# Optimization experiments

Measured on AMD Instinct MI355X. Metric: run time of the kernel, lower is better.

Reference implementation:

```python
import jax, jax.numpy as jnp
import numpy as np

B, MAXN, D, H, S = 64, 512, 512, 8, 32
DH = D // H          # per-head dim = 64
N = B * MAXN         # 32768 total nodes
E = 524288           # ~avg degree 16
EPS = 1e-5


def setup_inputs() -> dict:
    key = jax.random.key(0)
    ks = jax.random.split(key, 18)
    s = 0.05
    x_dense = jax.random.normal(ks[0], (B, MAXN, D), jnp.float32)
    x = jax.random.normal(ks[1], (N, D), jnp.float32)
    src = jax.random.randint(ks[2], (E,), 0, N)
    # destinations kept within the same graph as the source
    dst = (src // MAXN) * MAXN + jax.random.randint(ks[3], (E,), 0, MAXN)
    edge_index = jnp.stack([src, dst]).astype(jnp.int32)
    batch = (jnp.arange(N) // MAXN).astype(jnp.int32)  # sorted, 512 nodes/graph
    seed = jax.random.normal(ks[4], (S, 1, D), jnp.float32) * s
    # per-head GCN conv weights concatenated along output dim: [D, H*DH] == [D, D]
    Wk = jax.random.normal(ks[5], (D, D), jnp.float32) * s
    bk = jnp.zeros((D,), jnp.float32)
    Wv = jax.random.normal(ks[6], (D, D), jnp.float32) * s
    bv = jnp.zeros((D,), jnp.float32)
    q_proj_weight = jax.random.normal(ks[7], (D, D), jnp.float32) * s
    Wo = jax.random.normal(ks[8], (D, D), jnp.float32) * s
    bo = jnp.zeros((D,), jnp.float32)
    Wff = jax.random.normal(ks[9], (D, D), jnp.float32) * s
    bff = jnp.zeros((D,), jnp.float32)
    gamma_h = jnp.ones((D,), jnp.float32)
    beta_h = jnp.zeros((D,), jnp.float32)
    gamma_z = jnp.ones((D,), jnp.float32)
    beta_z = jnp.zeros((D,), jnp.float32)
    return dict(x_dense=x_dense, x=x, edge_index=edge_index, batch=batch,
                seed=seed, Wk=Wk, bk=bk, Wv=Wv, bv=bv,
                q_proj_weight=q_proj_weight, Wo=Wo, bo=bo, Wff=Wff, bff=bff,
                gamma_h=gamma_h, beta_h=beta_h, gamma_z=gamma_z, beta_z=beta_z)


def _gcn(x, W, b, src, dst):
    # PyG GCNConv with self-loops + symmetric norm; all H heads fused via W [D, H*DH]
    xw = x @ W                                   # [N, D]
    idx = jnp.arange(N)
    src_f = jnp.concatenate([src, idx])
    dst_f = jnp.concatenate([dst, idx])
    deg = jax.ops.segment_sum(jnp.ones_like(dst_f, dtype=x.dtype), dst_f, num_segments=N)
    dinv = jax.lax.rsqrt(deg)                    # deg >= 1 (self-loops)
    norm = dinv[src_f] * dinv[dst_f]             # [E+N]
    out = jax.ops.segment_sum(xw[src_f] * norm[:, None], dst_f, num_segments=N)
    return out + b


def _to_dense(feat, batch):
    # to_dense_batch for sorted batch vector; padded slots are zeros
    counts = jax.ops.segment_sum(jnp.ones((N,), jnp.int32), batch, num_segments=B)
    start = jnp.cumsum(counts) - counts
    pos = jnp.arange(N) - start[batch]
    return jnp.zeros((B, MAXN, feat.shape[-1]), feat.dtype).at[batch, pos].set(feat)


def _layernorm(x, g, b):
    m = jnp.mean(x, -1, keepdims=True)
    v = jnp.mean(jnp.square(x - m), -1, keepdims=True)
    return (x - m) * jax.lax.rsqrt(v + EPS) * g + b


def reference(x_dense, x, edge_index, batch, seed, Wk, bk, Wv, bv,
              q_proj_weight, Wo, bo, Wff, bff, gamma_h, beta_h, gamma_z, beta_z):
    src, dst = edge_index[0], edge_index[1]
    k_nodes = _gcn(x, Wk, bk, src, dst)          # [N, D] (H heads concat)
    v_nodes = _gcn(x, Wv, bv, src, dst)
    k_dense = _to_dense(k_nodes, batch)          # [B, MAXN, D]
    v_dense = _to_dense(v_nodes, batch)

    # query: seed [S,1,D] repeated over batch -> [S,B,D]; q projection (F.linear)
    query = jnp.broadcast_to(seed, (S, B, D))
    q = jnp.einsum('sbd,ed->sbe', query, q_proj_weight)
    scale = 1.0 / jnp.sqrt(jnp.float32(DH))
    qh = (q * scale).reshape(S, B, H, DH).transpose(1, 2, 0, 3)     # [B,H,S,DH]
    kh = k_dense.reshape(B, MAXN, H, DH).transpose(0, 2, 1, 3)      # [B,H,N,DH]
    vh = v_dense.reshape(B, MAXN, H, DH).transpose(0, 2, 1, 3)
    scores = jnp.einsum('bhsd,bhnd->bhsn', qh, kh)                  # [B,H,S,MAXN]
    attn = jax.nn.softmax(scores, axis=-1)                          # no padding mask (faithful)
    ctx = jnp.einsum('bhsn,bhnd->bhsd', attn, vh)                   # [B,H,S,DH]
    ctx = ctx.transpose(0, 2, 1, 3).reshape(B, S, D)                # heads concat
    attn_out = ctx @ Wo.T + bo                                      # [B,S,D]

    query_bse = jnp.broadcast_to(seed.transpose(1, 0, 2), (B, S, D))
    embed = _layernorm(query_bse + attn_out, gamma_h, beta_h)
    embed = _layernorm(embed + embed @ Wff.T + bff, gamma_z, beta_z)
    return embed
```

## Files before the change

kernel.cpp:

```cpp
#include <hip/hip_runtime.h>
#include <hip/hip_bf16.h>

#define BN   64
#define MAXN 512
#define DIM  512
#define NH   8
#define NS   32
#define NN   32768
#define NE   524288
#define NBLK 256
#define EPB  (NE / NBLK)
#define MP   (2048 * 512)

typedef __hip_bfloat16 bf16;
using bf16x8 = __attribute__((ext_vector_type(8))) short;
using f32x4  = __attribute__((ext_vector_type(4))) float;

__device__ int            g_cnt[NN];
__device__ int            g_off[NN + 1];
__device__ int            g_csr[NE];
__device__ unsigned short g_hist[(long)NBLK * NN];
__device__ unsigned short g_bpfx[(long)NBLK * NN];
__device__ float g_dinv[NN];
__device__ bf16  g_xb[NN * DIM];
__device__ bf16  g_agg[NN * DIM];
__device__ bf16  g_aggT[NN * DIM];
__device__ bf16  g_qf[256 * DIM];
__device__ bf16  g_wob[DIM * DIM];
__device__ bf16  g_wvb[DIM * DIM];
__device__ bf16  g_wvo[DIM * 8 * DIM];
__device__ float g_bvo[DIM];
__device__ bf16  g_wffT[DIM * DIM];
__device__ float g_q[NS * DIM];
__device__ bf16  g_sc[BN * 256 * MAXN];
__device__ bf16  g_cp[BN * NS * 8 * DIM];
__device__ float g_part[4 * MP];
__device__ float g_h1[BN * NS * DIM];
__device__ bf16  g_h1b[BN * NS * DIM];

__device__ inline float bf2f(unsigned short u) {
    union { unsigned int i; float f; } x; x.i = ((unsigned int)u) << 16; return x.f;
}

__device__ inline void gll16(const bf16* g, bf16* l) {
    __builtin_amdgcn_global_load_lds(
        (const __attribute__((address_space(1))) void*)g,
        (__attribute__((address_space(3))) void*)l, 16, 0, 0);
}

__global__ __launch_bounds__(1024) void k_hist(const int* __restrict__ dst) {
    __shared__ unsigned int h[NN];
    int p = blockIdx.x, tid = threadIdx.x;
    for (int i = tid; i < NN / 4; i += 1024) ((int4*)h)[i] = make_int4(0, 0, 0, 0);
    __syncthreads();
#pragma unroll
    for (int j = 0; j < EPB / 1024; j++) {
        int e = p * EPB + j * 1024 + tid;
        atomicAdd(&h[dst[e]], 1u);
    }
    __syncthreads();
    unsigned int* out32 = (unsigned int*)(g_hist + (long)p * NN);
    for (int i = tid; i < NN / 2; i += 1024)
        out32[i] = h[2 * i] | (h[2 * i + 1] << 16);
}

__global__ __launch_bounds__(256) void k_colscan() {
    int v2 = blockIdx.x * 256 + threadIdx.x;
    const unsigned int* H = (const unsigned int*)g_hist;
    unsigned int* B = (unsigned int*)g_bpfx;
    unsigned int s0 = 0, s1 = 0;
#pragma unroll 8
    for (int p = 0; p < NBLK; p++) {
        unsigned int hh = H[(long)p * (NN / 2) + v2];
        B[(long)p * (NN / 2) + v2] = s0 | (s1 << 16);
        s0 += hh & 0xffffu; s1 += hh >> 16;
    }
    g_cnt[2 * v2] = (int)s0;
    g_cnt[2 * v2 + 1] = (int)s1;
    g_dinv[2 * v2] = rsqrtf(1.0f + (float)s0);
    g_dinv[2 * v2 + 1] = rsqrtf(1.0f + (float)s1);
}

__global__ void k_scan() {
    __shared__ int part[1024];
    int t = threadIdx.x;
    int base = t * 32;
    int loc[32]; int s = 0;
#pragma unroll
    for (int i = 0; i < 32; i++) { loc[i] = g_cnt[base + i]; s += loc[i]; }
    part[t] = s; __syncthreads();
    for (int o = 1; o < 1024; o <<= 1) {
        int v = (t >= o) ? part[t - o] : 0;
        __syncthreads();
        part[t] += v;
        __syncthreads();
    }
    int ex = (t == 0) ? 0 : part[t - 1];
#pragma unroll
    for (int i = 0; i < 32; i++) { g_off[base + i] = ex; ex += loc[i]; }
    if (t == 1023) g_off[NN] = ex;
}

__global__ __launch_bounds__(1024) void k_fillsort(const int* __restrict__ src,
                                                   const int* __restrict__ dst) {
    __shared__ unsigned int l[NN];
    int p = blockIdx.x, tid = threadIdx.x;
    const unsigned int* bp32 = (const unsigned int*)(g_bpfx + (long)p * NN);
    for (int i = tid; i < NN / 2; i += 1024) {
        unsigned int v = bp32[i];
        ((uint2*)l)[i] = make_uint2(v & 0xffffu, v >> 16);
    }
    __syncthreads();
#pragma unroll
    for (int j = 0; j < EPB / 1024; j++) {
        int e = p * EPB + j * 1024 + tid;
        int v = dst[e];
        unsigned int r = atomicAdd(&l[v], 1u);
        g_csr[g_off[v] + r] = src[e];
    }
}

__global__ __launch_bounds__(256) void k_prep(const float* __restrict__ seed,
                                              const float* __restrict__ Wq,
                                              const float* __restrict__ Wo,
                                              const float* __restrict__ Wv,
                                              const float* __restrict__ Wff,
                                              const float* __restrict__ bo,
                                              const float* __restrict__ bv) {
    int blk = blockIdx.x;
    if (blk < 64) {
        int i = blk * 256 + threadIdx.x;
        int s = i >> 9, e = i & 511;
        const float* sr = seed + s * DIM;
        const float* wr = Wq + e * DIM;
        float a0 = 0.f, a1 = 0.f;
        for (int d = 0; d < DIM; d += 8) {
            float4 a = *(const float4*)(sr + d);
            float4 b = *(const float4*)(wr + d);
            float4 c = *(const float4*)(sr + d + 4);
            float4 w = *(const float4*)(wr + d + 4);
            a0 += a.x * b.x + a.y * b.y + a.z * b.z + a.w * b.w;
            a1 += c.x * w.x + c.y * w.y + c.z * w.z + c.w * w.w;
        }
        g_q[i] = (a0 + a1) * 0.125f;
    } else if (blk < 448) {
        long t = (long)(blk - 64) * 256 + threadIdx.x;
        const float* srcp; bf16* dstp; long off;
        if (t < 32768)      { srcp = Wo;  dstp = g_wob;  off = t; }
        else if (t < 65536) { srcp = Wv;  dstp = g_wvb;  off = t - 32768; }
        else                { srcp = Wff; dstp = g_wffT; off = t - 65536; }
        long i = off * 8;
        float4 a = *(const float4*)(srcp + i);
        float4 b = *(const float4*)(srcp + i + 4);
        float v[8] = {a.x, a.y, a.z, a.w, b.x, b.y, b.z, b.w};
        bf16x8 o;
#pragma unroll
        for (int j = 0; j < 8; j++) { bf16 q = __float2bfloat16(v[j]); o[j] = *(short*)&q; }
        *(bf16x8*)(dstp + i) = o;
    } else {
        int e = (blk - 448) * 256 + threadIdx.x;
        const float* orow = Wo + (long)e * DIM;
        float a0 = 0.f, a1 = 0.f;
        for (int c = 0; c < DIM; c += 8) {
            float4 a = *(const float4*)(bv + c);
            float4 w = *(const float4*)(orow + c);
            float4 xx = *(const float4*)(bv + c + 4);
            float4 u = *(const float4*)(orow + c + 4);
            a0 += a.x * w.x + a.y * w.y + a.z * w.z + a.w * w.w;
            a1 += xx.x * u.x + xx.y * u.y + xx.z * u.z + xx.w * u.w;
        }
        g_bvo[e] = bo[e] + a0 + a1;
    }
}

__device__ __forceinline__ void gemm128(const bf16* __restrict__ A, long lda,
                                        const bf16* __restrict__ Bt, long ldb,
                                        long row0, long col0, int kbeg, int kend,
                                        bf16 (*As)[128 * 32], bf16 (*Bs)[128 * 32],
                                        f32x4 acc[4][4]) {
    int tid = threadIdx.x;
    int lane = tid & 63, wave = tid >> 6;
    int wr = wave >> 1, wc = wave & 1;
    int fr = lane & 15, fq = lane >> 4;
    int rchunk = (fq ^ ((fr >> 1) & 3)) * 8;
    int u0 = wave * 128 + lane;
    int sr0 = u0 >> 2, sc0 = ((u0 & 3) ^ ((sr0 >> 1) & 3)) * 8;
    int u1 = u0 + 64;
    int sr1 = u1 >> 2, sc1 = ((u1 & 3) ^ ((sr1 >> 1) & 3)) * 8;

    auto stage = [&](int buf, int kt) {
        gll16(A + (row0 + sr0) * lda + kt + sc0, As[buf] + u0 * 8);
        gll16(A + (row0 + sr1) * lda + kt + sc1, As[buf] + u1 * 8);
        gll16(Bt + (col0 + sr0) * ldb + kt + sc0, Bs[buf] + u0 * 8);
        gll16(Bt + (col0 + sr1) * ldb + kt + sc1, Bs[buf] + u1 * 8);
    };

    stage(0, kbeg);
    __syncthreads();
    for (int kt = kbeg; kt < kend; kt += 32) {
        int buf = ((kt - kbeg) >> 5) & 1;
        if (kt + 32 < kend) stage(buf ^ 1, kt + 32);
        bf16x8 af[4], bfv[4];
#pragma unroll
        for (int mi = 0; mi < 4; mi++)
            af[mi] = *(const bf16x8*)(As[buf] + (wr * 64 + mi * 16 + fr) * 32 + rchunk);
#pragma unroll
        for (int ni = 0; ni < 4; ni++)
            bfv[ni] = *(const bf16x8*)(Bs[buf] + (wc * 64 + ni * 16 + fr) * 32 + rchunk);
#pragma unroll
        for (int mi = 0; mi < 4; mi++)
#pragma unroll
            for (int ni = 0; ni < 4; ni++)
                acc[mi][ni] = __builtin_amdgcn_mfma_f32_16x16x32_bf16(af[mi], bfv[ni], acc[mi][ni], 0, 0, 0);
        __syncthreads();
    }
}

#define ACC_INIT                                             \
    f32x4 acc[4][4];                                         \
    _Pragma("unroll")                                        \
    for (int i = 0; i < 4; i++)                              \
        _Pragma("unroll")                                    \
        for (int j = 0; j < 4; j++) acc[i][j] = (f32x4){0.f, 0.f, 0.f, 0.f}; \
    int lane = threadIdx.x & 63, wave = threadIdx.x >> 6;    \
    int wr = wave >> 1, wc = wave & 1;                       \
    int fr = lane & 15, fq = lane >> 4;

__global__ __launch_bounds__(256) void k_xbqf(const float* __restrict__ x,
                                              const float* __restrict__ Wk) {
    __shared__ bf16 As[2][128 * 32];
    __shared__ bf16 Bs[2][128 * 32];
    int blk = blockIdx.x;
    if (blk < 8192) {
        long i = (long)blk * (256 * 8) + (long)threadIdx.x * 8;
        int node = (int)(i >> 9);
        float w = g_dinv[node];
        float4 a = *(const float4*)(x + i);
        float4 b = *(const float4*)(x + i + 4);
        float v[8] = {a.x, a.y, a.z, a.w, b.x, b.y, b.z, b.w};
        bf16x8 o;
#pragma unroll
        for (int j = 0; j < 8; j++) { bf16 t = __float2bfloat16(v[j] * w); o[j] = *(short*)&t; }
        *(bf16x8*)(g_xb + i) = o;
    } else if (blk < 8704) {
        int i = (blk - 8192) * 256 + threadIdx.x;
        int hs = i >> 9, d = i & 511;
        int h = hs >> 5, s = hs & 31;
        const float* qr = g_q + s * DIM + h * 64;
        const float* wr = Wk + d * DIM + h * 64;
        float a0 = 0.f, a1 = 0.f;
        for (int t2 = 0; t2 < 64; t2 += 8) {
            float4 a = *(const float4*)(qr + t2);
            float4 w = *(const float4*)(wr + t2);
            float4 c = *(const float4*)(qr + t2 + 4);
            float4 u = *(const float4*)(wr + t2 + 4);
            a0 += a.x * w.x + a.y * w.y + a.z * w.z + a.w * w.w;
            a1 += c.x * u.x + c.y * u.y + c.z * u.z + c.w * u.w;
        }
        g_qf[i] = __float2bfloat16(a0 + a1);
    } else {
        int wi = blk - 8704;
        int bx = wi & 3, by = (wi >> 2) & 3, h = wi >> 4;
        ACC_INIT
        long row0 = (long)bx * 128, col0 = (long)by * 128;
        gemm128(g_wob, DIM, g_wvb, DIM, row0, col0, h * 64, h * 64 + 64, As, Bs, acc);
#pragma unroll
        for (int mi = 0; mi < 4; mi++)
#pragma unroll
            for (int ni = 0; ni < 4; ni++) {
                long col = col0 + wc * 64 + ni * 16 + fr;
#pragma unroll
                for (int r = 0; r < 4; r++) {
                    long row = row0 + wr * 64 + mi * 16 + fq * 4 + r;
                    g_wvo[row * 4096 + h * 512 + col] = __float2bfloat16(acc[mi][ni][r]);
                }
            }
    }
}

__global__ __launch_bounds__(256) void k_gather() {
    int bid = blockIdx.x;
    int lb = (bid & 7) * 1024 + (bid >> 3);
    int wave = threadIdx.x >> 6, lane = threadIdx.x & 63;
    int node = lb * 4 + wave;

    bf16x8 sv = ((const bf16x8*)(g_xb + (long)node * DIM))[lane];
    float acc[8];
#pragma unroll
    for (int j = 0; j < 8; j++) acc[j] = bf2f((unsigned short)sv[j]);

    int e = g_off[node], e1 = g_off[node + 1];
    for (; e + 8 <= e1; e += 8) {
        bf16x8 r[8];
#pragma unroll
        for (int q = 0; q < 8; q++)
            r[q] = ((const bf16x8*)(g_xb + (long)g_csr[e + q] * DIM))[lane];
#pragma unroll
        for (int j = 0; j < 8; j++) {
            float s01 = bf2f((unsigned short)r[0][j]) + bf2f((unsigned short)r[1][j]);
            float s23 = bf2f((unsigned short)r[2][j]) + bf2f((unsigned short)r[3][j]);
            float s45 = bf2f((unsigned short)r[4][j]) + bf2f((unsigned short)r[5][j]);
            float s67 = bf2f((unsigned short)r[6][j]) + bf2f((unsigned short)r[7][j]);
            acc[j] += (s01 + s23) + (s45 + s67);
        }
    }
    for (; e < e1; e++) {
        bf16x8 r0 = ((const bf16x8*)(g_xb + (long)g_csr[e] * DIM))[lane];
#pragma unroll
        for (int j = 0; j < 8; j++) acc[j] += bf2f((unsigned short)r0[j]);
    }
    float dd = g_dinv[node];
    bf16x8 o;
#pragma unroll
    for (int j = 0; j < 8; j++) { bf16 t = __float2bfloat16(acc[j] * dd); o[j] = *(short*)&t; }
    ((bf16x8*)(g_agg + (long)node * DIM))[lane] = o;
}

__global__ __launch_bounds__(256) void k_aggsc() {
    __shared__ __align__(16) char smem[32768];
    int blk = blockIdx.x;
    if (blk < 512) {
        bf16 (*As)[128 * 32] = (bf16(*)[128 * 32])smem;
        bf16 (*Bs)[128 * 32] = (bf16(*)[128 * 32])(smem + 16384);
        int b = blk & 63, bx = (blk >> 6) & 1, by = blk >> 7;
        ACC_INIT
        long row0 = (long)bx * 128, col0 = (long)by * 128;
        gemm128(g_qf, DIM, g_agg + (long)b * (MAXN * DIM), DIM, row0, col0, 0, DIM, As, Bs, acc);
        bf16* out = g_sc + (long)b * (256 * MAXN);
#pragma unroll
        for (int mi = 0; mi < 4; mi++)
#pragma unroll
            for (int ni = 0; ni < 4; ni++) {
                long col = col0 + wc * 64 + ni * 16 + fr;
#pragma unroll
                for (int r = 0; r < 4; r++) {
                    long row = row0 + wr * 64 + mi * 16 + fq * 4 + r;
                    out[row * MAXN + col] = __float2bfloat16(acc[mi][ni][r]);
                }
            }
    } else {
        unsigned short (*L)[72] = (unsigned short(*)[72])smem;
        int id = blk - 512;
        int b = id >> 6, t = id & 63;
        int n0 = (t & 7) * 64, d0 = (t >> 3) * 64;
        int tid = threadIdx.x;
        const unsigned short* src = (const unsigned short*)g_agg + ((long)b * 512 + n0) * 512 + d0;
#pragma unroll
        for (int p = 0; p < 2; p++) {
            int r = (tid >> 3) + 32 * p, c = (tid & 7) * 8;
            *(int4*)&L[r][c] = *(const int4*)(src + (long)r * 512 + c);
        }
        __syncthreads();
        unsigned short* dst = (unsigned short*)g_aggT + ((long)b * 512 + d0) * 512 + n0;
#pragma unroll
        for (int p = 0; p < 2; p++) {
            int dr = (tid >> 3) + 32 * p, c0 = (tid & 7) * 8;
            unsigned short tmp[8];
#pragma unroll
            for (int j = 0; j < 8; j++) tmp[j] = L[c0 + j][dr];
            *(int4*)(dst + (long)dr * 512 + c0) = *(int4*)tmp;
        }
    }
}

__global__ __launch_bounds__(256) void k_soft() {
    int w = threadIdx.x >> 6, lane = threadIdx.x & 63;
    unsigned short* base = (unsigned short*)g_sc + ((long)blockIdx.x * 16 + w * 4) * MAXN;
#pragma unroll
    for (int r = 0; r < 4; r++) {
        unsigned short* row = base + (long)r * MAXN;
        float v[8]; float m = -1e30f;
#pragma unroll
        for (int k = 0; k < 8; k++) { v[k] = bf2f(row[lane + 64 * k]); m = fmaxf(m, v[k]); }
#pragma unroll
        for (int o = 32; o > 0; o >>= 1) m = fmaxf(m, __shfl_xor(m, o));
        float sum = 0.f;
#pragma unroll
        for (int k = 0; k < 8; k++) { v[k] = __expf(v[k] - m); sum += v[k]; }
#pragma unroll
        for (int o = 32; o > 0; o >>= 1) sum += __shfl_xor(sum, o);
        float inv = 1.0f / sum;
#pragma unroll
        for (int k = 0; k < 8; k++) {
            bf16 t = __float2bfloat16(v[k] * inv);
            row[lane + 64 * k] = *(unsigned short*)&t;
        }
    }
}

__global__ __launch_bounds__(256) void k_pvg() {
    __shared__ bf16 As[2][128 * 32];
    __shared__ bf16 Bs[2][128 * 32];
    int blk = blockIdx.x;
    int b = blk & 63, bx = (blk >> 6) & 1, by = (blk >> 7) & 1, dh = blk >> 8;
    ACC_INIT
    long row0 = (long)bx * 128, col0 = (long)by * 128;
    gemm128(g_sc + (long)b * (256 * MAXN), MAXN,
            g_aggT + (long)b * (DIM * MAXN) + (long)dh * (256 * MAXN), MAXN,
            row0, col0, 0, MAXN, As, Bs, acc);
#pragma unroll
    for (int mi = 0; mi < 4; mi++)
#pragma unroll
        for (int ni = 0; ni < 4; ni++) {
            long col = col0 + wc * 64 + ni * 16 + fr;
#pragma unroll
            for (int r = 0; r < 4; r++) {
                long row = row0 + wr * 64 + mi * 16 + fq * 4 + r;
                g_cp[((long)b * NS + (row & 31)) * 4096 + (row >> 5) * 512 + dh * 256 + col] =
                    __float2bfloat16(acc[mi][ni][r]);
            }
        }
}

__global__ __launch_bounds__(256) void k_vo() {
    __shared__ bf16 As[2][128 * 32];
    __shared__ bf16 Bs[2][128 * 32];
    ACC_INIT
    int z = blockIdx.z;
    long row0 = (long)blockIdx.x * 128, col0 = (long)blockIdx.y * 128;
    gemm128(g_cp, 4096, g_wvo, 4096, row0, col0, z * 1024, z * 1024 + 1024, As, Bs, acc);
    float* out = g_part + (long)z * MP;
#pragma unroll
    for (int mi = 0; mi < 4; mi++)
#pragma unroll
        for (int ni = 0; ni < 4; ni++) {
            long col = col0 + wc * 64 + ni * 16 + fr;
#pragma unroll
            for (int r = 0; r < 4; r++) {
                long row = row0 + wr * 64 + mi * 16 + fq * 4 + r;
                out[row * DIM + col] = acc[mi][ni][r];
            }
        }
}

__global__ __launch_bounds__(256) void k_ffn() {
    __shared__ bf16 As[2][128 * 32];
    __shared__ bf16 Bs[2][128 * 32];
    ACC_INIT
    int z = blockIdx.z;
    long row0 = (long)blockIdx.x * 128, col0 = (long)blockIdx.y * 128;
    gemm128(g_h1b, DIM, g_wffT, DIM, row0, col0, z * 128, z * 128 + 128, As, Bs, acc);
    float* out = g_part + (long)z * MP;
#pragma unroll
    for (int mi = 0; mi < 4; mi++)
#pragma unroll
        for (int ni = 0; ni < 4; ni++) {
            long col = col0 + wc * 64 + ni * 16 + fr;
#pragma unroll
            for (int r = 0; r < 4; r++) {
                long row = row0 + wr * 64 + mi * 16 + fq * 4 + r;
                out[row * DIM + col] = acc[mi][ni][r];
            }
        }
}

__device__ inline float blockReduceSum(float v, float* red, int tid) {
#pragma unroll
    for (int o = 32; o > 0; o >>= 1) v += __shfl_xor(v, o);
    __syncthreads();
    if ((tid & 63) == 0) red[tid >> 6] = v;
    __syncthreads();
    return red[0] + red[1] + red[2] + red[3];
}

__global__ __launch_bounds__(256) void k_ln1(const float* __restrict__ seed,
                                             const float* __restrict__ gamma,
                                             const float* __restrict__ beta) {
    __shared__ float red[4];
    int r = blockIdx.x, t = threadIdx.x;
    int s = r & 31;
    long base = (long)r * DIM;
    float v0 = seed[s * DIM + t] + g_bvo[t];
    float v1 = seed[s * DIM + 256 + t] + g_bvo[256 + t];
#pragma unroll
    for (int z = 0; z < 4; z++) {
        v0 += g_part[(long)z * MP + base + t];
        v1 += g_part[(long)z * MP + base + 256 + t];
    }
    float mean = blockReduceSum(v0 + v1, red, t) * (1.0f / DIM);
    float d0 = v0 - mean, d1 = v1 - mean;
    float var = blockReduceSum(d0 * d0 + d1 * d1, red, t) * (1.0f / DIM);
    float ri = rsqrtf(var + 1e-5f);
    float o0 = d0 * ri * gamma[t] + beta[t];
    float o1 = d1 * ri * gamma[256 + t] + beta[256 + t];
    g_h1[base + t] = o0; g_h1[base + 256 + t] = o1;
    g_h1b[base + t] = __float2bfloat16(o0);
    g_h1b[base + 256 + t] = __float2bfloat16(o1);
}

__global__ __launch_bounds__(256) void k_ln2(const float* __restrict__ gamma,
                                             const float* __restrict__ beta,
                                             const float* __restrict__ bff,
                                             float* __restrict__ out) {
    __shared__ float red[4];
    int r = blockIdx.x, t = threadIdx.x;
    long base = (long)r * DIM;
    float v0 = g_h1[base + t] + bff[t];
    float v1 = g_h1[base + 256 + t] + bff[256 + t];
#pragma unroll
    for (int z = 0; z < 4; z++) {
        v0 += g_part[(long)z * MP + base + t];
        v1 += g_part[(long)z * MP + base + 256 + t];
    }
    float mean = blockReduceSum(v0 + v1, red, t) * (1.0f / DIM);
    float d0 = v0 - mean, d1 = v1 - mean;
    float var = blockReduceSum(d0 * d0 + d1 * d1, red, t) * (1.0f / DIM);
    float ri = rsqrtf(var + 1e-5f);
    out[base + t] = d0 * ri * gamma[t] + beta[t];
    out[base + 256 + t] = d1 * ri * gamma[256 + t] + beta[256 + t];
}

extern "C" void kernel_launch(void* const* d_in, const int* in_sizes, int n_in,
                              void* d_out, int out_size, void* d_ws, size_t ws_size,
                              hipStream_t stream) {
    (void)in_sizes; (void)n_in; (void)out_size; (void)d_ws; (void)ws_size;
    const float* x    = (const float*)d_in[1];
    const int*   ei   = (const int*)d_in[2];
    const int*   esrc = ei;
    const int*   edst = ei + NE;
    const float* seed = (const float*)d_in[4];
    const float* Wk   = (const float*)d_in[5];
    const float* Wv   = (const float*)d_in[7];
    const float* bv   = (const float*)d_in[8];
    const float* Wq   = (const float*)d_in[9];
    const float* Wo   = (const float*)d_in[10];
    const float* bo   = (const float*)d_in[11];
    const float* Wff  = (const float*)d_in[12];
    const float* bff  = (const float*)d_in[13];
    const float* gh   = (const float*)d_in[14];
    const float* bh   = (const float*)d_in[15];
    const float* gz   = (const float*)d_in[16];
    const float* bz   = (const float*)d_in[17];
    float* out = (float*)d_out;

    k_hist    <<<NBLK, 1024, 0, stream>>>(edst);
    k_colscan <<<NN / 512, 256, 0, stream>>>();
    k_scan    <<<1, 1024, 0, stream>>>();
    k_prep    <<<450, 256, 0, stream>>>(seed, Wq, Wo, Wv, Wff, bo, bv);
    k_fillsort<<<NBLK, 1024, 0, stream>>>(esrc, edst);
    k_xbqf    <<<8832, 256, 0, stream>>>(x, Wk);
    k_gather  <<<NN / 4, 256, 0, stream>>>();
    k_aggsc   <<<512 + BN * 64, 256, 0, stream>>>();
    k_soft    <<<1024, 256, 0, stream>>>();
    k_pvg     <<<512, 256, 0, stream>>>();
    k_vo      <<<dim3(16, 4, 4), 256, 0, stream>>>();
    k_ln1     <<<BN * NS, 256, 0, stream>>>(seed, gh, bh);
    k_ffn     <<<dim3(16, 4, 4), 256, 0, stream>>>();
    k_ln2     <<<BN * NS, 256, 0, stream>>>(gz, bz, bff, out);
}
```

Baseline: 221.2 us.

## Fuse aggregated-feature transpose into gather kernel via shared-memory tile

The gather kernel now handles 32 nodes per 1024-thread block. Each normalized output row is staged into a padded shared-memory tile and written back transposed to g_aggT. The separate transpose blocks in the score kernel are removed, so g_agg is no longer re-read from global memory just to transpose it. In exchange, gather blocks get larger and carry a barrier plus LDS pressure, and the score GEMM runs alone in its own launch.

```diff
diff --git a/kernel.cpp b/kernel.cpp
--- a/kernel.cpp
+++ b/kernel.cpp
@@ -278,89 +278,84 @@
     }
 }
 
-__global__ __launch_bounds__(256) void k_gather() {
+__global__ __launch_bounds__(1024) void k_gather3() {
+    __shared__ unsigned short T[512 * 33];
     int bid = blockIdx.x;
-    int lb = (bid & 7) * 1024 + (bid >> 3);
-    int wave = threadIdx.x >> 6, lane = threadIdx.x & 63;
-    int node = lb * 4 + wave;
-
-    bf16x8 sv = ((const bf16x8*)(g_xb + (long)node * DIM))[lane];
-    float acc[8];
-#pragma unroll
-    for (int j = 0; j < 8; j++) acc[j] = bf2f((unsigned short)sv[j]);
-
-    int e = g_off[node], e1 = g_off[node + 1];
-    for (; e + 8 <= e1; e += 8) {
-        bf16x8 r[8];
-#pragma unroll
-        for (int q = 0; q < 8; q++)
-            r[q] = ((const bf16x8*)(g_xb + (long)g_csr[e + q] * DIM))[lane];
+    int gb = (bid & 7) * 128 + (bid >> 3);
+    int b = gb >> 4, nt = gb & 15;
+    int w = threadIdx.x >> 6, lane = threadIdx.x & 63;
+
+#pragma unroll
+    for (int k = 0; k < 2; k++) {
+        int nl = w * 2 + k;
+        int node = b * 512 + nt * 32 + nl;
+
+        bf16x8 sv = ((const bf16x8*)(g_xb + (long)node * DIM))[lane];
+        float acc[8];
+#pragma unroll
+        for (int j = 0; j < 8; j++) acc[j] = bf2f((unsigned short)sv[j]);
+
+        int e = g_off[node], e1 = g_off[node + 1];
+        for (; e + 8 <= e1; e += 8) {
+            bf16x8 r[8];
+#pragma unroll
+            for (int q = 0; q < 8; q++)
+                r[q] = ((const bf16x8*)(g_xb + (long)g_csr[e + q] * DIM))[lane];
+#pragma unroll
+            for (int j = 0; j < 8; j++) {
+                float s01 = bf2f((unsigned short)r[0][j]) + bf2f((unsigned short)r[1][j]);
+                float s23 = bf2f((unsigned short)r[2][j]) + bf2f((unsigned short)r[3][j]);
+                float s45 = bf2f((unsigned short)r[4][j]) + bf2f((unsigned short)r[5][j]);
+                float s67 = bf2f((unsigned short)r[6][j]) + bf2f((unsigned short)r[7][j]);
+                acc[j] += (s01 + s23) + (s45 + s67);
+            }
+        }
+        for (; e < e1; e++) {
+            bf16x8 r0 = ((const bf16x8*)(g_xb + (long)g_csr[e] * DIM))[lane];
+#pragma unroll
+            for (int j = 0; j < 8; j++) acc[j] += bf2f((unsigned short)r0[j]);
+        }
+        float dd = g_dinv[node];
+        bf16x8 o;
 #pragma unroll
         for (int j = 0; j < 8; j++) {
-            float s01 = bf2f((unsigned short)r[0][j]) + bf2f((unsigned short)r[1][j]);
-            float s23 = bf2f((unsigned short)r[2][j]) + bf2f((unsigned short)r[3][j]);
-            float s45 = bf2f((unsigned short)r[4][j]) + bf2f((unsigned short)r[5][j]);
-            float s67 = bf2f((unsigned short)r[6][j]) + bf2f((unsigned short)r[7][j]);
-            acc[j] += (s01 + s23) + (s45 + s67);
-        }
-    }
-    for (; e < e1; e++) {
-        bf16x8 r0 = ((const bf16x8*)(g_xb + (long)g_csr[e] * DIM))[lane];
-#pragma unroll
-        for (int j = 0; j < 8; j++) acc[j] += bf2f((unsigned short)r0[j]);
-    }
-    float dd = g_dinv[node];
-    bf16x8 o;
-#pragma unroll
-    for (int j = 0; j < 8; j++) { bf16 t = __float2bfloat16(acc[j] * dd); o[j] = *(short*)&t; }
-    ((bf16x8*)(g_agg + (long)node * DIM))[lane] = o;
-}
-
-__global__ __launch_bounds__(256) void k_aggsc() {
-    __shared__ __align__(16) char smem[32768];
+            bf16 t = __float2bfloat16(acc[j] * dd);
+            o[j] = *(short*)&t;
+            T[(lane * 8 + j) * 33 + nl] = *(unsigned short*)&t;
+        }
+        ((bf16x8*)(g_agg + (long)node * DIM))[lane] = o;
+    }
+    __syncthreads();
+
+    int f = threadIdx.x >> 1, half = threadIdx.x & 1;
+    unsigned short tmp[16];
+#pragma unroll
+    for (int j = 0; j < 16; j++) tmp[j] = T[f * 33 + half * 16 + j];
+    unsigned short* dst = (unsigned short*)g_aggT + ((long)b * 512 + f) * 512 + nt * 32 + half * 16;
+    *(int4*)dst = *(int4*)tmp;
+    *(int4*)(dst + 8) = *(int4*)(tmp + 8);
+}
+
+__global__ __launch_bounds__(256) void k_score() {
+    __shared__ bf16 As[2][128 * 32];
+    __shared__ bf16 Bs[2][128 * 32];
     int blk = blockIdx.x;
-    if (blk < 512) {
-        bf16 (*As)[128 * 32] = (bf16(*)[128 * 32])smem;
-        bf16 (*Bs)[128 * 32] = (bf16(*)[128 * 32])(smem + 16384);
-        int b = blk & 63, bx = (blk >> 6) & 1, by = blk >> 7;
-        ACC_INIT
-        long row0 = (long)bx * 128, col0 = (long)by * 128;
-        gemm128(g_qf, DIM, g_agg + (long)b * (MAXN * DIM), DIM, row0, col0, 0, DIM, As, Bs, acc);
-        bf16* out = g_sc + (long)b * (256 * MAXN);
-#pragma unroll
-        for (int mi = 0; mi < 4; mi++)
-#pragma unroll
-            for (int ni = 0; ni < 4; ni++) {
-                long col = col0 + wc * 64 + ni * 16 + fr;
-#pragma unroll
-                for (int r = 0; r < 4; r++) {
-                    long row = row0 + wr * 64 + mi * 16 + fq * 4 + r;
-                    out[row * MAXN + col] = __float2bfloat16(acc[mi][ni][r]);
-                }
+    int b = blk & 63, bx = (blk >> 6) & 1, by = blk >> 7;
+    ACC_INIT
+    long row0 = (long)bx * 128, col0 = (long)by * 128;
+    gemm128(g_qf, DIM, g_agg + (long)b * (MAXN * DIM), DIM, row0, col0, 0, DIM, As, Bs, acc);
+    bf16* out = g_sc + (long)b * (256 * MAXN);
+#pragma unroll
+    for (int mi = 0; mi < 4; mi++)
+#pragma unroll
+        for (int ni = 0; ni < 4; ni++) {
+            long col = col0 + wc * 64 + ni * 16 + fr;
+#pragma unroll
+            for (int r = 0; r < 4; r++) {
+                long row = row0 + wr * 64 + mi * 16 + fq * 4 + r;
+                out[row * MAXN + col] = __float2bfloat16(acc[mi][ni][r]);
             }
-    } else {
-        unsigned short (*L)[72] = (unsigned short(*)[72])smem;
-        int id = blk - 512;
-        int b = id >> 6, t = id & 63;
-        int n0 = (t & 7) * 64, d0 = (t >> 3) * 64;
-        int tid = threadIdx.x;
-        const unsigned short* src = (const unsigned short*)g_agg + ((long)b * 512 + n0) * 512 + d0;
-#pragma unroll
-        for (int p = 0; p < 2; p++) {
-            int r = (tid >> 3) + 32 * p, c = (tid & 7) * 8;
-            *(int4*)&L[r][c] = *(const int4*)(src + (long)r * 512 + c);
-        }
-        __syncthreads();
-        unsigned short* dst = (unsigned short*)g_aggT + ((long)b * 512 + d0) * 512 + n0;
-#pragma unroll
-        for (int p = 0; p < 2; p++) {
-            int dr = (tid >> 3) + 32 * p, c0 = (tid & 7) * 8;
-            unsigned short tmp[8];
-#pragma unroll
-            for (int j = 0; j < 8; j++) tmp[j] = L[c0 + j][dr];
-            *(int4*)(dst + (long)dr * 512 + c0) = *(int4*)tmp;
-        }
-    }
+        }
 }
 
 __global__ __launch_bounds__(256) void k_soft() {
@@ -539,8 +534,8 @@
     k_prep    <<<450, 256, 0, stream>>>(seed, Wq, Wo, Wv, Wff, bo, bv);
     k_fillsort<<<NBLK, 1024, 0, stream>>>(esrc, edst);
     k_xbqf    <<<8832, 256, 0, stream>>>(x, Wk);
-    k_gather  <<<NN / 4, 256, 0, stream>>>();
-    k_aggsc   <<<512 + BN * 64, 256, 0, stream>>>();
+    k_gather3 <<<1024, 1024, 0, stream>>>();
+    k_score   <<<512, 256, 0, stream>>>();
     k_soft    <<<1024, 256, 0, stream>>>();
     k_pvg     <<<512, 256, 0, stream>>>();
     k_vo      <<<dim3(16, 4, 4), 256, 0, stream>>>();
```

After: 220.9 us. Within noise of the previous version (-0.1%).
